# Optimization experiments

Hardware: AMD Instinct MI355X
Metric: run time of the kernel (lower is better)

Reference implementation:

```python
import jax, jax.numpy as jnp
import numpy as np

B, L, D = 32, 4096, 768
WINDOW = 32
LN_EPS = 1e-5


def setup_inputs() -> dict:
    key = jax.random.key(0)
    k1, k2, k3 = jax.random.split(key, 3)
    ref_repr = jax.random.normal(k1, (B, L, D), dtype=jnp.float32)
    alt_repr = jax.random.normal(k2, (B, L, D), dtype=jnp.float32)
    variant_pos = jax.random.randint(k3, (B,), 0, L, dtype=jnp.int64)
    gamma = jnp.ones((D,), dtype=jnp.float32)
    beta = jnp.zeros((D,), dtype=jnp.float32)
    return {"ref_repr": ref_repr, "alt_repr": alt_repr, "variant_pos": variant_pos,
            "gamma": gamma, "beta": beta}


def reference(ref_repr, alt_repr, variant_pos, gamma, beta):
    b, l, d = ref_repr.shape
    w = WINDOW
    offs = jnp.arange(-w, w + 1)                      # [2w+1]
    idx = variant_pos[:, None] + offs[None, :]        # [B, 2w+1] raw window indices
    valid = (idx >= 0) & (idx < l)                    # boundary mask (clamped window)
    idx_c = jnp.clip(idx, 0, l - 1)
    bidx = jnp.arange(b)[:, None]
    # gather only the windows, not the full sequence: [B, 2w+1, D]
    diff = alt_repr[bidx, idx_c] - ref_repr[bidx, idx_c]
    m = valid[..., None].astype(diff.dtype)
    count = valid.sum(axis=1, keepdims=True).astype(diff.dtype)  # [B,1]
    pooled = (diff * m).sum(axis=1) / count           # [B, D] masked mean over window
    # LayerNorm over D (biased variance, like nn.LayerNorm)
    mu = pooled.mean(axis=-1, keepdims=True)
    var = jnp.mean((pooled - mu) ** 2, axis=-1, keepdims=True)
    return (pooled - mu) * jax.lax.rsqrt(var + LN_EPS) * gamma + beta
```

## Files before the change

### kernel.cpp

```cpp
#include <hip/hip_runtime.h>

#define BATCH 32
#define SEQL 4096
#define DIM 768
#define D4 192
#define WIN 32
#define NPOS 65
#define CHUNKS 13
#define PERCHUNK 5
#define LN_EPS 1e-5f

__global__ __launch_bounds__(D4) void pool_partial_kernel(
    const float4* __restrict__ refv, const float4* __restrict__ altv,
    const int* __restrict__ pos, float4* __restrict__ wsv) {
  const int b = blockIdx.y;
  const int chunk = blockIdx.x;
  const int tid = threadIdx.x;
  const int p0 = pos[b] - WIN + chunk * PERCHUNK;

  float4 acc = make_float4(0.f, 0.f, 0.f, 0.f);
#pragma unroll
  for (int i = 0; i < PERCHUNK; ++i) {
    const int p = p0 + i;
    if (p >= 0 && p < SEQL) {
      const size_t off = ((size_t)b * SEQL + p) * D4 + tid;
      const float4 a = altv[off];
      const float4 r = refv[off];
      acc.x += a.x - r.x;
      acc.y += a.y - r.y;
      acc.z += a.z - r.z;
      acc.w += a.w - r.w;
    }
  }
  wsv[((size_t)b * CHUNKS + chunk) * D4 + tid] = acc;
}

__global__ __launch_bounds__(D4) void ln_kernel(
    const float4* __restrict__ wsv, const int* __restrict__ pos,
    const float4* __restrict__ gammav, const float4* __restrict__ betav,
    float4* __restrict__ outv) {
  const int b = blockIdx.x;
  const int tid = threadIdx.x;

  const int p = pos[b];
  const int lo = (p - WIN) > 0 ? (p - WIN) : 0;
  const int hi = (p + WIN) < (SEQL - 1) ? (p + WIN) : (SEQL - 1);
  const float inv_cnt = 1.f / (float)(hi - lo + 1);

  float4 s = make_float4(0.f, 0.f, 0.f, 0.f);
#pragma unroll
  for (int c = 0; c < CHUNKS; ++c) {
    const float4 v = wsv[((size_t)b * CHUNKS + c) * D4 + tid];
    s.x += v.x; s.y += v.y; s.z += v.z; s.w += v.w;
  }
  s.x *= inv_cnt; s.y *= inv_cnt; s.z *= inv_cnt; s.w *= inv_cnt;

  float lsum = s.x + s.y + s.z + s.w;
  float lsq  = s.x * s.x + s.y * s.y + s.z * s.z + s.w * s.w;

#pragma unroll
  for (int off = 32; off > 0; off >>= 1) {
    lsum += __shfl_down(lsum, off);
    lsq  += __shfl_down(lsq, off);
  }

  __shared__ float sh[6];
  const int wave = tid >> 6;
  if ((tid & 63) == 0) {
    sh[wave] = lsum;
    sh[3 + wave] = lsq;
  }
  __syncthreads();

  const float tot   = sh[0] + sh[1] + sh[2];
  const float totsq = sh[3] + sh[4] + sh[5];
  const float mu  = tot * (1.f / (float)DIM);
  const float var = totsq * (1.f / (float)DIM) - mu * mu;
  const float rstd = rsqrtf(var + LN_EPS);

  const float4 g  = gammav[tid];
  const float4 bb = betav[tid];
  float4 o;
  o.x = (s.x - mu) * rstd * g.x + bb.x;
  o.y = (s.y - mu) * rstd * g.y + bb.y;
  o.z = (s.z - mu) * rstd * g.z + bb.z;
  o.w = (s.w - mu) * rstd * g.w + bb.w;
  outv[(size_t)b * D4 + tid] = o;
}

extern "C" void kernel_launch(void* const* d_in, const int* in_sizes, int n_in,
                              void* d_out, int out_size, void* d_ws, size_t ws_size,
                              hipStream_t stream) {
  const float* ref_repr = (const float*)d_in[0];
  const float* alt_repr = (const float*)d_in[1];
  const int*   vpos     = (const int*)d_in[2];
  const float* gamma    = (const float*)d_in[3];
  const float* beta     = (const float*)d_in[4];
  float* out = (float*)d_out;
  float* ws  = (float*)d_ws;

  dim3 gridA(CHUNKS, BATCH);
  pool_partial_kernel<<<gridA, D4, 0, stream>>>(
      (const float4*)ref_repr, (const float4*)alt_repr, vpos, (float4*)ws);

  ln_kernel<<<BATCH, D4, 0, stream>>>(
      (const float4*)ws, vpos, (const float4*)gamma, (const float4*)beta,
      (float4*)out);
}
```

Baseline: 583.6 us.

## Fuse window pooling and LayerNorm into a single per-batch kernel

Merges the two-kernel pipeline (partial window sums written to a workspace, then a LayerNorm kernel) into one kernel with one 960-thread block per batch row. Five thread groups each sum 13 window positions, reduce through shared memory, and then the first 192 threads run the LayerNorm. This removes the second launch and the global workspace round trip. In exchange the grid shrinks from 416 blocks to 32, so far fewer loads are in flight across the device, and the LN phase leaves most threads idle.

```diff
diff --git a/kernel.cpp b/kernel.cpp
--- a/kernel.cpp
+++ b/kernel.cpp
@@ -6,24 +6,30 @@
 #define D4 192
 #define WIN 32
 #define NPOS 65
-#define CHUNKS 13
-#define PERCHUNK 5
+#define GROUPS 5
+#define PERGRP 13
+#define BLK (GROUPS * D4)
 #define LN_EPS 1e-5f
 
-__global__ __launch_bounds__(D4) void pool_partial_kernel(
+__global__ __launch_bounds__(BLK) void fused_pool_ln_kernel(
     const float4* __restrict__ refv, const float4* __restrict__ altv,
-    const int* __restrict__ pos, float4* __restrict__ wsv) {
-  const int b = blockIdx.y;
-  const int chunk = blockIdx.x;
+    const int* __restrict__ pos,
+    const float4* __restrict__ gammav, const float4* __restrict__ betav,
+    float4* __restrict__ outv) {
+  const int b   = blockIdx.x;
   const int tid = threadIdx.x;
-  const int p0 = pos[b] - WIN + chunk * PERCHUNK;
+  const int g   = tid / D4;
+  const int t   = tid % D4;
+
+  const int p  = pos[b];
+  const int p0 = p - WIN + g * PERGRP;
 
   float4 acc = make_float4(0.f, 0.f, 0.f, 0.f);
 #pragma unroll
-  for (int i = 0; i < PERCHUNK; ++i) {
-    const int p = p0 + i;
-    if (p >= 0 && p < SEQL) {
-      const size_t off = ((size_t)b * SEQL + p) * D4 + tid;
+  for (int i = 0; i < PERGRP; ++i) {
+    const int q = p0 + i;
+    if (q >= 0 && q < SEQL) {
+      const size_t off = ((size_t)b * SEQL + q) * D4 + t;
       const float4 a = altv[off];
       const float4 r = refv[off];
       acc.x += a.x - r.x;
@@ -32,60 +38,56 @@
       acc.w += a.w - r.w;
     }
   }
-  wsv[((size_t)b * CHUNKS + chunk) * D4 + tid] = acc;
-}
 
-__global__ __launch_bounds__(D4) void ln_kernel(
-    const float4* __restrict__ wsv, const int* __restrict__ pos,
-    const float4* __restrict__ gammav, const float4* __restrict__ betav,
-    float4* __restrict__ outv) {
-  const int b = blockIdx.x;
-  const int tid = threadIdx.x;
-
-  const int p = pos[b];
-  const int lo = (p - WIN) > 0 ? (p - WIN) : 0;
-  const int hi = (p + WIN) < (SEQL - 1) ? (p + WIN) : (SEQL - 1);
-  const float inv_cnt = 1.f / (float)(hi - lo + 1);
+  __shared__ float4 sh[BLK];
+  __shared__ float  sh2[6];
+  sh[tid] = acc;
+  __syncthreads();
 
   float4 s = make_float4(0.f, 0.f, 0.f, 0.f);
+  if (tid < D4) {
+    s = sh[t];
 #pragma unroll
-  for (int c = 0; c < CHUNKS; ++c) {
-    const float4 v = wsv[((size_t)b * CHUNKS + c) * D4 + tid];
-    s.x += v.x; s.y += v.y; s.z += v.z; s.w += v.w;
-  }
-  s.x *= inv_cnt; s.y *= inv_cnt; s.z *= inv_cnt; s.w *= inv_cnt;
+    for (int gg = 1; gg < GROUPS; ++gg) {
+      const float4 v = sh[gg * D4 + t];
+      s.x += v.x; s.y += v.y; s.z += v.z; s.w += v.w;
+    }
+    const int lo = (p - WIN) > 0 ? (p - WIN) : 0;
+    const int hi = (p + WIN) < (SEQL - 1) ? (p + WIN) : (SEQL - 1);
+    const float inv_cnt = 1.f / (float)(hi - lo + 1);
+    s.x *= inv_cnt; s.y *= inv_cnt; s.z *= inv_cnt; s.w *= inv_cnt;
 
-  float lsum = s.x + s.y + s.z + s.w;
-  float lsq  = s.x * s.x + s.y * s.y + s.z * s.z + s.w * s.w;
-
+    float lsum = s.x + s.y + s.z + s.w;
+    float lsq  = s.x * s.x + s.y * s.y + s.z * s.z + s.w * s.w;
 #pragma unroll
-  for (int off = 32; off > 0; off >>= 1) {
-    lsum += __shfl_down(lsum, off);
-    lsq  += __shfl_down(lsq, off);
-  }
-
-  __shared__ float sh[6];
-  const int wave = tid >> 6;
-  if ((tid & 63) == 0) {
-    sh[wave] = lsum;
-    sh[3 + wave] = lsq;
+    for (int off = 32; off > 0; off >>= 1) {
+      lsum += __shfl_down(lsum, off);
+      lsq  += __shfl_down(lsq, off);
+    }
+    const int wave = tid >> 6;
+    if ((tid & 63) == 0) {
+      sh2[wave]     = lsum;
+      sh2[3 + wave] = lsq;
+    }
   }
   __syncthreads();
 
-  const float tot   = sh[0] + sh[1] + sh[2];
-  const float totsq = sh[3] + sh[4] + sh[5];
-  const float mu  = tot * (1.f / (float)DIM);
-  const float var = totsq * (1.f / (float)DIM) - mu * mu;
-  const float rstd = rsqrtf(var + LN_EPS);
+  if (tid < D4) {
+    const float tot   = sh2[0] + sh2[1] + sh2[2];
+    const float totsq = sh2[3] + sh2[4] + sh2[5];
+    const float mu   = tot * (1.f / (float)DIM);
+    const float var  = totsq * (1.f / (float)DIM) - mu * mu;
+    const float rstd = rsqrtf(var + LN_EPS);
 
-  const float4 g  = gammav[tid];
-  const float4 bb = betav[tid];
-  float4 o;
-  o.x = (s.x - mu) * rstd * g.x + bb.x;
-  o.y = (s.y - mu) * rstd * g.y + bb.y;
-  o.z = (s.z - mu) * rstd * g.z + bb.z;
-  o.w = (s.w - mu) * rstd * g.w + bb.w;
-  outv[(size_t)b * D4 + tid] = o;
+    const float4 gm = gammav[t];
+    const float4 bt = betav[t];
+    float4 o;
+    o.x = (s.x - mu) * rstd * gm.x + bt.x;
+    o.y = (s.y - mu) * rstd * gm.y + bt.y;
+    o.z = (s.z - mu) * rstd * gm.z + bt.z;
+    o.w = (s.w - mu) * rstd * gm.w + bt.w;
+    outv[(size_t)b * D4 + t] = o;
+  }
 }
 
 extern "C" void kernel_launch(void* const* d_in, const int* in_sizes, int n_in,
@@ -97,13 +99,9 @@
   const float* gamma    = (const float*)d_in[3];
   const float* beta     = (const float*)d_in[4];
   float* out = (float*)d_out;
-  float* ws  = (float*)d_ws;
+  (void)d_ws; (void)ws_size;
 
-  dim3 gridA(CHUNKS, BATCH);
-  pool_partial_kernel<<<gridA, D4, 0, stream>>>(
-      (const float4*)ref_repr, (const float4*)alt_repr, vpos, (float4*)ws);
-
-  ln_kernel<<<BATCH, D4, 0, stream>>>(
-      (const float4*)ws, vpos, (const float4*)gamma, (const float4*)beta,
-      (float4*)out);
+  fused_pool_ln_kernel<<<BATCH, BLK, 0, stream>>>(
+      (const float4*)ref_repr, (const float4*)alt_repr, vpos,
+      (const float4*)gamma, (const float4*)beta, (float4*)out);
 }
```

After: 591.0 us. Within noise of the previous version (+1.3%).
